# Kernel tuning notes

Hardware: AMD Instinct MI355X
Metric: run time of the kernel (lower is better)

Reference implementation:

```python
import jax, jax.numpy as jnp
import numpy as np

B, S, D = 2, 1024, 5120
NH, NKV, HD = 80, 8, 128
GROUPS = NH // NKV
SCALE = HD ** -0.5
ROPE_THETA = 1.0e7


def setup_inputs() -> dict:
    key = jax.random.key(0)
    ks = jax.random.split(key, 8)
    hidden_states = jax.random.normal(ks[0], (B, S, D), dtype=jnp.float32)
    # real RoPE tables from rope_theta (default rope_type)
    inv_freq = 1.0 / (ROPE_THETA ** (np.arange(0, HD, 2, dtype=np.float32) / HD))  # [HD/2]
    pos = np.arange(S, dtype=np.float32)
    freqs = np.outer(pos, inv_freq)                      # [S, HD/2]
    emb = np.concatenate([freqs, freqs], axis=-1)        # [S, HD]
    cos = jnp.asarray(np.broadcast_to(np.cos(emb), (B, S, HD)).copy())
    sin = jnp.asarray(np.broadcast_to(np.sin(emb), (B, S, HD)).copy())
    w_scale = 0.02
    q_w = jax.random.normal(ks[1], (NH * HD, D), dtype=jnp.float32) * w_scale
    q_b = jax.random.normal(ks[2], (NH * HD,), dtype=jnp.float32) * w_scale
    k_w = jax.random.normal(ks[3], (NKV * HD, D), dtype=jnp.float32) * w_scale
    k_b = jax.random.normal(ks[4], (NKV * HD,), dtype=jnp.float32) * w_scale
    v_w = jax.random.normal(ks[5], (NKV * HD, D), dtype=jnp.float32) * w_scale
    v_b = jax.random.normal(ks[6], (NKV * HD,), dtype=jnp.float32) * w_scale
    o_w = jax.random.normal(ks[7], (D, NH * HD), dtype=jnp.float32) * w_scale
    return dict(hidden_states=hidden_states, cos=cos, sin=sin,
                q_w=q_w, q_b=q_b, k_w=k_w, k_b=k_b, v_w=v_w, v_b=v_b, o_w=o_w)


def _rotate_half(x):
    x1, x2 = jnp.split(x, 2, axis=-1)
    return jnp.concatenate([-x2, x1], axis=-1)


def reference(hidden_states, cos, sin, q_w, q_b, k_w, k_b, v_w, v_b, o_w):
    b, s, _ = hidden_states.shape
    # QKV projections (bias on q/k/v per attention_bias=True)
    q = (hidden_states @ q_w.T + q_b).reshape(b, s, NH, HD).transpose(0, 2, 1, 3)   # [b,NH,s,hd]
    k = (hidden_states @ k_w.T + k_b).reshape(b, s, NKV, HD).transpose(0, 2, 1, 3)  # [b,NKV,s,hd]
    v = (hidden_states @ v_w.T + v_b).reshape(b, s, NKV, HD).transpose(0, 2, 1, 3)
    # RoPE (rotate_half form); cos/sin broadcast over head dim
    c = cos[:, None, :, :]
    sn = sin[:, None, :, :]
    q = q * c + _rotate_half(q) * sn
    k = k * c + _rotate_half(k) * sn
    # GQA: repeat kv heads to match query heads
    k = jnp.repeat(k, GROUPS, axis=1)  # [b,NH,s,hd]
    v = jnp.repeat(v, GROUPS, axis=1)
    scores = jnp.einsum('bhqd,bhkd->bhqk', q, k) * SCALE
    causal = jnp.tril(jnp.ones((s, s), dtype=bool))
    scores = jnp.where(causal[None, None], scores, jnp.finfo(scores.dtype).min)
    attn = jax.nn.softmax(scores, axis=-1)
    out = jnp.einsum('bhqk,bhkd->bhqd', attn, v)                 # [b,NH,s,hd]
    out = out.transpose(0, 2, 1, 3).reshape(b, s, NH * HD)
    return out @ o_w.T                                           # o_proj, no bias
```

## Files before the change

### kernel.cpp

```cpp
#include <hip/hip_runtime.h>
#include <hip/hip_bf16.h>

#define NH 80
#define NKV 8
#define HD 128
#define GROUPS 10
#define SEQ 1024
#define BATCH 2
#define DMODEL 5120
#define NQKV 12288
#define MROWS 2048
#define QCOLS 10240
#define KOFF 10240
#define VOFF 11264
#define ATTN_SCALE 0.08838834764831845f

typedef __attribute__((ext_vector_type(8))) __bf16 bf16x8;
typedef __attribute__((ext_vector_type(4))) float f32x4;

__device__ inline unsigned short f2bf(float f) {
  unsigned u = __float_as_uint(f);
  u = (u + 0x7fffu + ((u >> 16) & 1u)) >> 16;
  return (unsigned short)u;
}
__device__ inline float bf2f(unsigned short h) {
  return __uint_as_float(((unsigned)h) << 16);
}

template <typename T>
__device__ inline T ld_vec(const void* p) {
  T v;
  __builtin_memcpy(&v, p, sizeof(T));
  return v;
}

__device__ inline void gload_lds16(const void* g, void* l) {
  __builtin_amdgcn_global_load_lds(
      (const __attribute__((address_space(1))) void*)g,
      (__attribute__((address_space(3))) void*)l, 16, 0, 0);
}

__global__ __launch_bounds__(256) void cvt_f32_bf16(
    const float* __restrict__ src, unsigned short* __restrict__ dst, long n) {
  long i = ((long)blockIdx.x * 256 + threadIdx.x) * 8;
  if (i + 8 > n) return;
  float4 a = *reinterpret_cast<const float4*>(src + i);
  float4 b = *reinterpret_cast<const float4*>(src + i + 4);
  union { unsigned short u[8]; uint4 v; } r;
  r.u[0] = f2bf(a.x); r.u[1] = f2bf(a.y); r.u[2] = f2bf(a.z); r.u[3] = f2bf(a.w);
  r.u[4] = f2bf(b.x); r.u[5] = f2bf(b.y); r.u[6] = f2bf(b.z); r.u[7] = f2bf(b.w);
  *reinterpret_cast<uint4*>(dst + i) = r.v;
}

__global__ __launch_bounds__(256) void concat_bias(
    const float* __restrict__ qb, const float* __restrict__ kb,
    const float* __restrict__ vb, float* __restrict__ out) {
  int i = blockIdx.x * 256 + threadIdx.x;
  if (i >= NQKV) return;
  float v;
  if (i < KOFF) v = qb[i];
  else if (i < VOFF) v = kb[i - KOFF];
  else v = vb[i - VOFF];
  out[i] = v;
}

template <int OUT_BF16, int HAS_BIAS>
__global__ __launch_bounds__(256, 4) void gemm_bt64(
    const unsigned short* __restrict__ A, const unsigned short* __restrict__ W,
    const float* __restrict__ bias, void* __restrict__ Cout,
    int M, int N, int K) {
  __shared__ unsigned short As[128 * 64];
  __shared__ unsigned short Bs[128 * 64];
  const int t = threadIdx.x;
  const int lane = t & 63, wave = t >> 6;
  const int m0 = blockIdx.y * 128, n0 = blockIdx.x * 128;
  const int wr = (wave >> 1) * 64, wc = (wave & 1) * 64;
  const int lr = lane & 15, lg = lane >> 4;
  int st_row[4], st_col[4];
#pragma unroll
  for (int ch = 0; ch < 4; ++ch) {
    int ol = wave * 1024 + ch * 4096 + lane * 16;
    int row = ol >> 7, cb = ol & 127;
    st_row[ch] = row;
    st_col[ch] = cb ^ ((row & 7) << 4);
  }
  f32x4 acc[4][4] = {};
  const int swz = (lr & 7) << 4;
  for (int k0 = 0; k0 < K; k0 += 64) {
#pragma unroll
    for (int ch = 0; ch < 4; ++ch) {
      int od = wave * 1024 + ch * 4096;
      gload_lds16((const char*)A +
                      ((size_t)(m0 + st_row[ch]) * K + k0) * 2 + st_col[ch],
                  (char*)As + od);
      gload_lds16((const char*)W +
                      ((size_t)(n0 + st_row[ch]) * K + k0) * 2 + st_col[ch],
                  (char*)Bs + od);
    }
    __syncthreads();
    bf16x8 af[4][2], bfr[4][2];
#pragma unroll
    for (int ks = 0; ks < 2; ++ks) {
      int colb = (ks * 64 + lg * 16) ^ swz;
#pragma unroll
      for (int m = 0; m < 4; ++m)
        af[m][ks] =
            ld_vec<bf16x8>((const char*)As + (wr + m * 16 + lr) * 128 + colb);
#pragma unroll
      for (int n = 0; n < 4; ++n)
        bfr[n][ks] =
            ld_vec<bf16x8>((const char*)Bs + (wc + n * 16 + lr) * 128 + colb);
    }
#pragma unroll
    for (int ks = 0; ks < 2; ++ks)
#pragma unroll
      for (int m = 0; m < 4; ++m)
#pragma unroll
        for (int n = 0; n < 4; ++n)
          acc[m][n] = __builtin_amdgcn_mfma_f32_16x16x32_bf16(
              af[m][ks], bfr[n][ks], acc[m][n], 0, 0, 0);
    __syncthreads();
  }
#pragma unroll
  for (int n = 0; n < 4; ++n) {
    int col = n0 + wc + n * 16 + lr;
    float bv = HAS_BIAS ? bias[col] : 0.0f;
#pragma unroll
    for (int m = 0; m < 4; ++m) {
#pragma unroll
      for (int r = 0; r < 4; ++r) {
        int row = m0 + wr + m * 16 + lg * 4 + r;
        float v = acc[m][n][r] + bv;
        if (OUT_BF16)
          ((unsigned short*)Cout)[(size_t)row * N + col] = f2bf(v);
        else
          ((float*)Cout)[(size_t)row * N + col] = v;
      }
    }
  }
}

__global__ __launch_bounds__(256) void rope_kernel(
    unsigned short* __restrict__ qkv, const float* __restrict__ cs,
    const float* __restrict__ sn) {
  int idx = blockIdx.x * 256 + threadIdx.x;
  int quad = idx & 15;
  int rest = idx >> 4;
  int slot = rest % 88;
  int row = rest / 88;
  if (row >= MROWS) return;
  int col = slot < NH ? slot * HD : KOFF + (slot - NH) * HD;
  unsigned short* p = qkv + (size_t)row * NQKV + col;
  const float* cp = cs + (size_t)row * HD;
  const float* sp = sn + (size_t)row * HD;
  int d0 = quad * 4;
  float4 c1 = *reinterpret_cast<const float4*>(cp + d0);
  float4 s1 = *reinterpret_cast<const float4*>(sp + d0);
  float4 c2 = *reinterpret_cast<const float4*>(cp + d0 + 64);
  float4 s2 = *reinterpret_cast<const float4*>(sp + d0 + 64);
  ushort4 x1 = *reinterpret_cast<const ushort4*>(p + d0);
  ushort4 x2 = *reinterpret_cast<const ushort4*>(p + d0 + 64);
  ushort4 o1, o2;
  float a, b;
  a = bf2f(x1.x); b = bf2f(x2.x);
  o1.x = f2bf(a * c1.x - b * s1.x); o2.x = f2bf(b * c2.x + a * s2.x);
  a = bf2f(x1.y); b = bf2f(x2.y);
  o1.y = f2bf(a * c1.y - b * s1.y); o2.y = f2bf(b * c2.y + a * s2.y);
  a = bf2f(x1.z); b = bf2f(x2.z);
  o1.z = f2bf(a * c1.z - b * s1.z); o2.z = f2bf(b * c2.z + a * s2.z);
  a = bf2f(x1.w); b = bf2f(x2.w);
  o1.w = f2bf(a * c1.w - b * s1.w); o2.w = f2bf(b * c2.w + a * s2.w);
  *reinterpret_cast<ushort4*>(p + d0) = o1;
  *reinterpret_cast<ushort4*>(p + d0 + 64) = o2;
}

__global__ __launch_bounds__(256, 2) void attn_kernel(
    const unsigned short* __restrict__ qkv, unsigned short* __restrict__ out) {
  __shared__ unsigned short Ks[64][128];
  __shared__ unsigned short Vt[128][64];
  __shared__ unsigned short Ps[4][32][72];
  const int t = threadIdx.x, lane = t & 63, wave = t >> 6;
  const int lr = lane & 15, lg = lane >> 4;
  const int blk = blockIdx.x;
  const int qt = 7 - blk / 160;
  const int bh = blk % 160;
  const int h = bh % NH, b = bh / NH;
  const int kvh = h / GROUPS;
  const int q0 = qt * 128;
  const int wrow0 = q0 + wave * 32;
  const unsigned short* Qb = qkv + (size_t)(b * SEQ) * NQKV + h * HD;
  const unsigned short* Kb = qkv + (size_t)(b * SEQ) * NQKV + KOFF + kvh * HD;
  const unsigned short* Vb = qkv + (size_t)(b * SEQ) * NQKV + VOFF + kvh * HD;
  int kst_row[4], kst_col[4];
#pragma unroll
  for (int ch = 0; ch < 4; ++ch) {
    int ol = wave * 1024 + ch * 4096 + lane * 16;
    int row = ol >> 8, cbyte = ol & 255;
    kst_row[ch] = row;
    kst_col[ch] = cbyte ^ ((row & 7) << 4);
  }
  bf16x8 qf[2][4];
#pragma unroll
  for (int rb = 0; rb < 2; ++rb)
#pragma unroll
    for (int kk = 0; kk < 4; ++kk)
      qf[rb][kk] = ld_vec<bf16x8>(Qb + (size_t)(wrow0 + rb * 16 + lr) * NQKV +
                                  kk * 32 + lg * 8);
  f32x4 acc[2][8] = {};
  float mrow[2][4], lrow[2][4];
#pragma unroll
  for (int rb = 0; rb < 2; ++rb)
#pragma unroll
    for (int r = 0; r < 4; ++r) { mrow[rb][r] = -__builtin_inff(); lrow[rb][r] = 0.f; }

  const int ntile = (q0 + 128) >> 6;
  for (int tt = 0; tt < ntile; ++tt) {
    const int kv0 = tt * 64;
    __syncthreads();
#pragma unroll
    for (int ch = 0; ch < 4; ++ch) {
      int od = wave * 1024 + ch * 4096;
      gload_lds16((const char*)Kb + ((size_t)(kv0 + kst_row[ch]) * NQKV) * 2 +
                      kst_col[ch],
                  (char*)&Ks[0][0] + od);
    }
#pragma unroll
    for (int i = 0; i < 4; ++i) {
      int e = i * 2048 + t * 8;
      int row = e >> 7, colc = e & 127;
      uint4 dv = ld_vec<uint4>(Vb + (size_t)(kv0 + row) * NQKV + colc);
      const unsigned short* pv = reinterpret_cast<const unsigned short*>(&dv);
#pragma unroll
      for (int j = 0; j < 8; ++j) {
        int dd = colc + j;
        int gp = ((row >> 3) + dd + (dd >> 3)) & 7;
        Vt[dd][(gp << 3) | (row & 7)] = pv[j];
      }
    }
    __syncthreads();
    if (kv0 > wrow0 + 31) continue;
    const bool needMask = (kv0 + 63) > wrow0;
#pragma unroll
    for (int rb = 0; rb < 2; ++rb) {
      f32x4 sf[4] = {};
#pragma unroll
      for (int kk = 0; kk < 4; ++kk) {
#pragma unroll
        for (int cb = 0; cb < 4; ++cb) {
          bf16x8 kfr = ld_vec<bf16x8>(
              (const char*)&Ks[0][0] + (cb * 16 + lr) * 256 +
              ((kk * 64 + lg * 16) ^ ((lr & 7) << 4)));
          sf[cb] = __builtin_amdgcn_mfma_f32_16x16x32_bf16(qf[rb][kk], kfr,
                                                           sf[cb], 0, 0, 0);
        }
      }
#pragma unroll
      for (int r = 0; r < 4; ++r) {
        int qrow = wrow0 + rb * 16 + lg * 4 + r;
        float mx = -3.0e38f;
#pragma unroll
        for (int cb = 0; cb < 4; ++cb) {
          float s = sf[cb][r] * ATTN_SCALE;
          if (needMask && (kv0 + cb * 16 + lr) > qrow) s = -__builtin_inff();
          sf[cb][r] = s;
          mx = fmaxf(mx, s);
        }
        mx = fmaxf(mx, __shfl_xor(mx, 1));
        mx = fmaxf(mx, __shfl_xor(mx, 2));
        mx = fmaxf(mx, __shfl_xor(mx, 4));
        mx = fmaxf(mx, __shfl_xor(mx, 8));
        float mold = mrow[rb][r];
        float mnew = fmaxf(mold, mx);
        float sfac = __expf(mold - mnew);
        mrow[rb][r] = mnew;
        float ps = 0.f;
#pragma unroll
        for (int cb = 0; cb < 4; ++cb) {
          float p = __expf(sf[cb][r] - mnew);
          ps += p;
          Ps[wave][rb * 16 + lg * 4 + r][cb * 16 + lr] = f2bf(p);
        }
        ps += __shfl_xor(ps, 1);
        ps += __shfl_xor(ps, 2);
        ps += __shfl_xor(ps, 4);
        ps += __shfl_xor(ps, 8);
        lrow[rb][r] = lrow[rb][r] * sfac + ps;
#pragma unroll
        for (int n = 0; n < 8; ++n) acc[rb][n][r] *= sfac;
      }
    }
#pragma unroll
    for (int kk = 0; kk < 2; ++kk) {
      bf16x8 vf[8];
#pragma unroll
      for (int cb = 0; cb < 8; ++cb) {
        int dd = cb * 16 + lr;
        int gp = (kk * 4 + lg + dd + (dd >> 3)) & 7;
        vf[cb] = ld_vec<bf16x8>(&Vt[dd][gp << 3]);
      }
#pragma unroll
      for (int rb = 0; rb < 2; ++rb) {
        bf16x8 pa = ld_vec<bf16x8>(&Ps[wave][rb * 16 + lr][kk * 32 + lg * 8]);
#pragma unroll
        for (int cb = 0; cb < 8; ++cb)
          acc[rb][cb] = __builtin_amdgcn_mfma_f32_16x16x32_bf16(pa, vf[cb],
                                                                acc[rb][cb], 0, 0, 0);
      }
    }
  }
#pragma unroll
  for (int rb = 0; rb < 2; ++rb)
#pragma unroll
    for (int n = 0; n < 8; ++n)
#pragma unroll
      for (int r = 0; r < 4; ++r) {
        int qrow = wrow0 + rb * 16 + lg * 4 + r;
        float v = acc[rb][n][r] / lrow[rb][r];
        out[(size_t)(b * SEQ + qrow) * QCOLS + h * HD + n * 16 + lr] = f2bf(v);
      }
}

extern "C" void kernel_launch(void* const* d_in, const int* in_sizes, int n_in,
                              void* d_out, int out_size, void* d_ws,
                              size_t ws_size, hipStream_t stream) {
  const float* hs   = (const float*)d_in[0];
  const float* cosb = (const float*)d_in[1];
  const float* sinb = (const float*)d_in[2];
  const float* q_w  = (const float*)d_in[3];
  const float* q_b  = (const float*)d_in[4];
  const float* k_w  = (const float*)d_in[5];
  const float* k_b  = (const float*)d_in[6];
  const float* v_w  = (const float*)d_in[7];
  const float* v_b  = (const float*)d_in[8];
  const float* o_w  = (const float*)d_in[9];

  char* ws = (char*)d_ws;
  unsigned short* hsB  = (unsigned short*)(ws);
  unsigned short* wqkv = (unsigned short*)(ws + 20971520ll);
  unsigned short* wo   = (unsigned short*)(ws + 146800640ll);
  unsigned short* qkv  = (unsigned short*)(ws + 251658240ll);
  unsigned short* attn = (unsigned short*)(ws + 301989888ll);
  float* bqkv          = (float*)(ws + 343932928ll);

  cvt_f32_bf16<<<dim3(5120), dim3(256), 0, stream>>>(hs, hsB, (long)MROWS * DMODEL);
  cvt_f32_bf16<<<dim3(25600), dim3(256), 0, stream>>>(q_w, wqkv, (long)QCOLS * DMODEL);
  cvt_f32_bf16<<<dim3(2560), dim3(256), 0, stream>>>(
      k_w, wqkv + (size_t)KOFF * DMODEL, (long)1024 * DMODEL);
  cvt_f32_bf16<<<dim3(2560), dim3(256), 0, stream>>>(
      v_w, wqkv + (size_t)VOFF * DMODEL, (long)1024 * DMODEL);
  cvt_f32_bf16<<<dim3(25600), dim3(256), 0, stream>>>(o_w, wo, (long)5120 * 10240);
  concat_bias<<<dim3(48), dim3(256), 0, stream>>>(q_b, k_b, v_b, bqkv);

  gemm_bt64<1, 1><<<dim3(96, 16), dim3(256), 0, stream>>>(
      hsB, wqkv, bqkv, qkv, MROWS, NQKV, DMODEL);
  rope_kernel<<<dim3(11264), dim3(256), 0, stream>>>(qkv, cosb, sinb);
  attn_kernel<<<dim3(1280), dim3(256), 0, stream>>>(qkv, attn);
  gemm_bt64<0, 0><<<dim3(40, 16), dim3(256), 0, stream>>>(
      attn, wo, nullptr, d_out, MROWS, 5120, 10240);
}
```

Baseline: 803.3 us.

## Use two-wave GEMM blocks with 64x128 per-wave tiles

Restructures the bf16 GEMM so each 128x128 block runs with 2 waves instead of 4. Each wave now computes a 64x128 sub-tile with 32 accumulator fragments, processing B fragments in two halves. The aim is more MFMA work per LDS load of A and fewer waves sharing each tile. In exchange it raises register pressure and roughly halves the waves available per CU to hide load latency.

```diff
diff --git a/kernel.cpp b/kernel.cpp
--- a/kernel.cpp
+++ b/kernel.cpp
@@ -65,7 +65,7 @@
 }
 
 template <int OUT_BF16, int HAS_BIAS>
-__global__ __launch_bounds__(256, 4) void gemm_bt64(
+__global__ __launch_bounds__(128, 2) void gemm_w128(
     const unsigned short* __restrict__ A, const unsigned short* __restrict__ W,
     const float* __restrict__ bias, void* __restrict__ Cout,
     int M, int N, int K) {
@@ -74,22 +74,21 @@
   const int t = threadIdx.x;
   const int lane = t & 63, wave = t >> 6;
   const int m0 = blockIdx.y * 128, n0 = blockIdx.x * 128;
-  const int wr = (wave >> 1) * 64, wc = (wave & 1) * 64;
   const int lr = lane & 15, lg = lane >> 4;
-  int st_row[4], st_col[4];
-#pragma unroll
-  for (int ch = 0; ch < 4; ++ch) {
-    int ol = wave * 1024 + ch * 4096 + lane * 16;
+  int st_row[8], st_col[8];
+#pragma unroll
+  for (int ch = 0; ch < 8; ++ch) {
+    int ol = ch * 2048 + wave * 1024 + lane * 16;
     int row = ol >> 7, cb = ol & 127;
     st_row[ch] = row;
     st_col[ch] = cb ^ ((row & 7) << 4);
   }
-  f32x4 acc[4][4] = {};
+  f32x4 acc[4][8] = {};
   const int swz = (lr & 7) << 4;
   for (int k0 = 0; k0 < K; k0 += 64) {
 #pragma unroll
-    for (int ch = 0; ch < 4; ++ch) {
-      int od = wave * 1024 + ch * 4096;
+    for (int ch = 0; ch < 8; ++ch) {
+      int od = ch * 2048 + wave * 1024;
       gload_lds16((const char*)A +
                       ((size_t)(m0 + st_row[ch]) * K + k0) * 2 + st_col[ch],
                   (char*)As + od);
@@ -98,39 +97,47 @@
                   (char*)Bs + od);
     }
     __syncthreads();
-    bf16x8 af[4][2], bfr[4][2];
+    bf16x8 af[4][2];
 #pragma unroll
     for (int ks = 0; ks < 2; ++ks) {
       int colb = (ks * 64 + lg * 16) ^ swz;
 #pragma unroll
       for (int m = 0; m < 4; ++m)
-        af[m][ks] =
-            ld_vec<bf16x8>((const char*)As + (wr + m * 16 + lr) * 128 + colb);
-#pragma unroll
-      for (int n = 0; n < 4; ++n)
-        bfr[n][ks] =
-            ld_vec<bf16x8>((const char*)Bs + (wc + n * 16 + lr) * 128 + colb);
-    }
-#pragma unroll
-    for (int ks = 0; ks < 2; ++ks)
-#pragma unroll
-      for (int m = 0; m < 4; ++m)
+        af[m][ks] = ld_vec<bf16x8>((const char*)As +
+                                   (wave * 64 + m * 16 + lr) * 128 + colb);
+    }
+#pragma unroll
+    for (int nh = 0; nh < 2; ++nh) {
+      bf16x8 bfr[4][2];
+#pragma unroll
+      for (int ks = 0; ks < 2; ++ks) {
+        int colb = (ks * 64 + lg * 16) ^ swz;
 #pragma unroll
         for (int n = 0; n < 4; ++n)
-          acc[m][n] = __builtin_amdgcn_mfma_f32_16x16x32_bf16(
-              af[m][ks], bfr[n][ks], acc[m][n], 0, 0, 0);
+          bfr[n][ks] = ld_vec<bf16x8>((const char*)Bs +
+                                      (nh * 64 + n * 16 + lr) * 128 + colb);
+      }
+#pragma unroll
+      for (int ks = 0; ks < 2; ++ks)
+#pragma unroll
+        for (int m = 0; m < 4; ++m)
+#pragma unroll
+          for (int n = 0; n < 4; ++n)
+            acc[m][nh * 4 + n] = __builtin_amdgcn_mfma_f32_16x16x32_bf16(
+                af[m][ks], bfr[n][ks], acc[m][nh * 4 + n], 0, 0, 0);
+    }
     __syncthreads();
   }
 #pragma unroll
-  for (int n = 0; n < 4; ++n) {
-    int col = n0 + wc + n * 16 + lr;
+  for (int j = 0; j < 8; ++j) {
+    int col = n0 + j * 16 + lr;
     float bv = HAS_BIAS ? bias[col] : 0.0f;
 #pragma unroll
     for (int m = 0; m < 4; ++m) {
 #pragma unroll
       for (int r = 0; r < 4; ++r) {
-        int row = m0 + wr + m * 16 + lg * 4 + r;
-        float v = acc[m][n][r] + bv;
+        int row = m0 + wave * 64 + m * 16 + lg * 4 + r;
+        float v = acc[m][j][r] + bv;
         if (OUT_BF16)
           ((unsigned short*)Cout)[(size_t)row * N + col] = f2bf(v);
         else
@@ -351,10 +358,10 @@
   cvt_f32_bf16<<<dim3(25600), dim3(256), 0, stream>>>(o_w, wo, (long)5120 * 10240);
   concat_bias<<<dim3(48), dim3(256), 0, stream>>>(q_b, k_b, v_b, bqkv);
 
-  gemm_bt64<1, 1><<<dim3(96, 16), dim3(256), 0, stream>>>(
+  gemm_w128<1, 1><<<dim3(96, 16), dim3(128), 0, stream>>>(
       hsB, wqkv, bqkv, qkv, MROWS, NQKV, DMODEL);
   rope_kernel<<<dim3(11264), dim3(256), 0, stream>>>(qkv, cosb, sinb);
   attn_kernel<<<dim3(1280), dim3(256), 0, stream>>>(qkv, attn);
-  gemm_bt64<0, 0><<<dim3(40, 16), dim3(256), 0, stream>>>(
+  gemm_w128<0, 0><<<dim3(40, 16), dim3(128), 0, stream>>>(
       attn, wo, nullptr, d_out, MROWS, 5120, 10240);
 }
```

Measured after the change: 850.5 us. 1.06x slower.
